# Kernel tuning notes

Hardware: AMD Instinct MI355X
Metric: run time of the kernel (lower is better)

The kernel has to match this reference:

```python
import jax, jax.numpy as jnp
import numpy as np

B, T, F = 32, 64, 128          # batch, time_steps, input_dim
H = 8                           # feat_dim (GRU hidden, MHA embed)
NH, HD = 4, 2                   # num_heads, head_dim
HID = 32                        # hidden_dim (out_proj out-features)


def setup_inputs() -> dict:
    key = jax.random.key(0)
    ks = jax.random.split(key, 16)
    s = 0.1
    inp = {
        'x': jax.random.normal(ks[0], (B, T, F), jnp.float32),
        # input_proj: Linear(F, F)
        'Wp': jax.random.normal(ks[1], (F, F), jnp.float32) * s,
        'bp': jax.random.normal(ks[2], (F,), jnp.float32) * s,
        # per-feature GRU weights stacked over F (input size 1 -> squeeze)
        'W_ih': jax.random.normal(ks[3], (F, 3 * H), jnp.float32) * s,
        'b_ih': jax.random.normal(ks[4], (F, 3 * H), jnp.float32) * s,
        'W_hh': jax.random.normal(ks[5], (F, 3 * H, H), jnp.float32) * s,
        'b_hh': jax.random.normal(ks[6], (F, 3 * H), jnp.float32) * s,
        # shared MultiheadAttention (embed=H, heads=NH)
        'in_w': jax.random.normal(ks[7], (3 * H, H), jnp.float32) * s,
        'in_b': jax.random.normal(ks[8], (3 * H,), jnp.float32) * s,
        'ow': jax.random.normal(ks[9], (H, H), jnp.float32) * s,
        'ob': jax.random.normal(ks[10], (H,), jnp.float32) * s,
        # out_proj: Linear(F*H, HID)
        'Wout': jax.random.normal(ks[11], (HID, F * H), jnp.float32) * s,
        'bout': jax.random.normal(ks[12], (HID,), jnp.float32) * s,
    }
    return inp


def _forward(x, Wp, bp, W_ih, b_ih, W_hh, b_hh, in_w, in_b, ow, ob, Wout, bout):
    xp = x @ Wp.T + bp                               # [B,T,F] input_proj

    # ---- batched per-feature GRU (vectorized over B and F, scan over T) ----
    def step(h, x_t):                                # h [B,F,H], x_t [B,F]
        gx = x_t[..., None] * W_ih + b_ih            # [B,F,3H]
        gh = jnp.einsum('bfh,fgh->bfg', h, W_hh) + b_hh
        r = jax.nn.sigmoid(gx[..., :H] + gh[..., :H])
        z = jax.nn.sigmoid(gx[..., H:2 * H] + gh[..., H:2 * H])
        n = jnp.tanh(gx[..., 2 * H:] + r * gh[..., 2 * H:])
        h_new = (1.0 - z) * n + z * h
        return h_new, h_new

    h0 = jnp.zeros((x.shape[0], F, H), x.dtype)
    _, hs = jax.lax.scan(step, h0, jnp.moveaxis(xp, 1, 0))   # [T,B,F,H]
    out = jnp.moveaxis(hs, 0, 1)                              # [B,T,F,H]

    # ---- shared MHA over time, batched across (B, F) ----
    seq = out.transpose(0, 2, 1, 3)                           # [B,F,T,H]
    qkv = seq @ in_w.T + in_b                                 # [B,F,T,3H]
    q, k, v = jnp.split(qkv, 3, axis=-1)
    def heads(t):  # [B,F,T,H] -> [B,F,T,NH,HD]
        return t.reshape(t.shape[:-1] + (NH, HD))
    q, k, v = heads(q), heads(k), heads(v)
    scale = 1.0 / np.sqrt(HD)
    scores = jnp.einsum('bfqnd,bfknd->bfnqk', q, k) * scale   # [B,F,NH,T,T]
    w = jax.nn.softmax(scores, axis=-1)
    ctx = jnp.einsum('bfnqk,bfknd->bfqnd', w, v)
    ctx = ctx.reshape(ctx.shape[:2] + (ctx.shape[2], H))      # [B,F,T,H]
    attn_out = ctx @ ow.T + ob                                # [B,F,T,H]
    attention = attn_out.transpose(0, 2, 1, 3)                # [B,T,F,H]

    # ---- flatten GRU outputs and project ----
    y = out.reshape(out.shape[0], out.shape[1], F * H) @ Wout.T + bout  # [B,T,HID]
    return y, attention


def reference(x, Wp, bp, W_ih, b_ih, W_hh, b_hh, in_w, in_b, ow, ob, Wout, bout):
    return _forward(x, Wp, bp, W_ih, b_ih, W_hh, b_hh, in_w, in_b, ow, ob, Wout, bout)
```

## Files before the change

### kernel.cpp

```cpp
#include <hip/hip_runtime.h>


namespace {
constexpr int Bb = 32, Tt = 64, Ff = 128, Hh = 8, HIDh = 32;
constexpr int G3H = 24;
constexpr float L2E = 1.44269504088896340736f;
constexpr int XS_STRIDE = 130;
constexpr int XP_OFF = Tt * XS_STRIDE;
constexpr int SMEM_AB = XP_OFF + 8 * 65;
constexpr int KK0 = 0, KK1 = 272, VV0 = 544, VV1 = 816, QS = 1088;
constexpr int WREG = 1728;
constexpr int OCT = 4 * WREG;
constexpr int SMEM_MHA = OCT + 4 * 640;
}

__device__ __forceinline__ float rcp_(float x) {
#if __has_builtin(__builtin_amdgcn_rcpf)
  return __builtin_amdgcn_rcpf(x);
#else
  return 1.0f / x;
#endif
}
__device__ __forceinline__ float exp2_(float x) {
#if __has_builtin(__builtin_amdgcn_exp2f)
  return __builtin_amdgcn_exp2f(x);
#else
  return exp2f(x);
#endif
}

__global__ __launch_bounds__(256) void k_gruproj(
    const float* __restrict__ x, const float* __restrict__ Wp, const float* __restrict__ bp,
    const float* __restrict__ W_ih, const float* __restrict__ b_ih,
    const float* __restrict__ W_hh, const float* __restrict__ b_hh,
    float* __restrict__ outp) {
  __shared__ float smem[SMEM_AB];
  const int tid = threadIdx.x;
  const int blk = blockIdx.x;
  const int b = blk >> 4;
  const int f0 = (blk & 15) * 8;
  const int lane = tid & 63;
  const int w = tid >> 6;

  {
    const float2* xb = (const float2*)(x + b * Tt * Ff);
    for (int i = tid; i < Tt * Ff / 2; i += 256) {
      int row = i >> 6, col2 = i & 63;
      *(float2*)&smem[row * XS_STRIDE + col2 * 2] = xb[i];
    }
  }
  __syncthreads();
  {
    const int t = lane;
    const int fA = f0 + w, fB = f0 + w + 4;
    float acc0 = bp[fA], acc1 = bp[fB];
    const float* wA = Wp + fA * Ff;
    const float* wB = Wp + fB * Ff;
    const float* xr = &smem[t * XS_STRIDE];
#pragma unroll 8
    for (int k = 0; k < Ff; k += 2) {
      float2 xv = *(const float2*)&xr[k];
      acc0 = fmaf(xv.x, wA[k], acc0); acc0 = fmaf(xv.y, wA[k + 1], acc0);
      acc1 = fmaf(xv.x, wB[k], acc1); acc1 = fmaf(xv.y, wB[k + 1], acc1);
    }
    smem[XP_OFF + w * 65 + t] = acc0;
    smem[XP_OFF + (w + 4) * 65 + t] = acc1;
  }
  __syncthreads();
  if (tid >= 64) return;

  {
    const int g = tid >> 3, j = tid & 7;
    const int f = f0 + g;
    const float* wb = W_hh + (f * G3H + j) * Hh;
    const float nL = -L2E, S2 = 2.0f * L2E;
    float w0s[8], w1s[8], w2s[8];
#pragma unroll
    for (int h = 0; h < 8; ++h) {
      w0s[h] = wb[h] * nL;
      w1s[h] = wb[64 + h] * nL;
      w2s[h] = wb[128 + h] * S2;
    }
    const float wi0s = W_ih[f * G3H + j] * nL;
    const float wi1s = W_ih[f * G3H + 8 + j] * nL;
    const float wi2s = W_ih[f * G3H + 16 + j] * S2;
    const float bias_r = (b_ih[f * G3H + j] + b_hh[f * G3H + j]) * nL;
    const float bias_z = (b_ih[f * G3H + 8 + j] + b_hh[f * G3H + 8 + j]) * nL;
    const float bi2s = b_ih[f * G3H + 16 + j] * S2;
    const float bh2s = b_hh[f * G3H + 16 + j] * S2;
    float hall[8];
#pragma unroll
    for (int h = 0; h < 8; ++h) hall[h] = 0.f;
    const int base = tid & 56;
    float* hdst = &smem[g * 520 + j * 65];
    const float* xps = &smem[XP_OFF + g * 65];
    for (int t = 0; t < Tt; ++t) {
      float xt = xps[t];
      float a0 = bias_r, a1 = bias_z, a2 = bh2s;
#pragma unroll
      for (int h = 0; h < 8; ++h) {
        a0 = fmaf(hall[h], w0s[h], a0);
        a1 = fmaf(hall[h], w1s[h], a1);
        a2 = fmaf(hall[h], w2s[h], a2);
      }
      float r = rcp_(1.0f + exp2_(fmaf(xt, wi0s, a0)));
      float z = rcp_(1.0f + exp2_(fmaf(xt, wi1s, a1)));
      float narg = fmaf(r, a2, fmaf(xt, wi2s, bi2s));
      float n = fmaf(-2.0f, rcp_(exp2_(narg) + 1.0f), 1.0f);
      float hn = fmaf(z, hall[j] - n, n);
      hdst[t] = hn;
#pragma unroll
      for (int h = 0; h < 8; ++h) hall[h] = __shfl(hn, base + h, 64);
    }
  }
  {
    float4* og = (float4*)(outp + (b * Ff + f0) * Tt * Hh);
#pragma unroll
    for (int i = 0; i < 16; ++i) {
      int v = i * 64 + tid;
      int g = v >> 7;
      int rem = v & 127;
      int t = rem >> 1, j0 = (rem & 1) * 4;
      const float* hp = &smem[g * 520 + j0 * 65 + t];
      og[v] = make_float4(hp[0], hp[65], hp[130], hp[195]);
    }
  }
}

#define MHA_STEP(K0C, K1C, V0C, V1C)                         \
  {                                                          \
    _Pragma("unroll") for (int i = 0; i < 4; ++i) {          \
      float s = fmaf(q0[i], K0C, q1[i] * K1C);               \
      float p = exp2_(s);                                    \
      ps[i] += p;                                            \
      c0[i] = fmaf(p, V0C, c0[i]);                           \
      c1[i] = fmaf(p, V1C, c1[i]);                           \
    }                                                        \
  }

__global__ __launch_bounds__(256) void k_mha_outproj(
    const float* __restrict__ outp, const float* __restrict__ in_w,
    const float* __restrict__ in_b, const float* __restrict__ ow,
    const float* __restrict__ ob, const float* __restrict__ Wout,
    const float* __restrict__ bout, float* __restrict__ attn,
    float* __restrict__ y) {
  __shared__ float smem[SMEM_MHA];
  const int tid = threadIdx.x;
  if (blockIdx.x < 1024) {
    const int wv = tid >> 6;
    const int t = tid & 63;
    const int pair = blockIdx.x * 4 + wv;
    float* sm = &smem[wv * WREG];

    const float4* src = (const float4*)(outp + pair * (Tt * Hh));
    float4 r0 = src[t * 2], r1 = src[t * 2 + 1];
    float sq[8] = {r0.x, r0.y, r0.z, r0.w, r1.x, r1.y, r1.z, r1.w};
    constexpr float SCL = 0.70710678118654752f * L2E;
    float qv[8], ka[8], va[8];
#pragma unroll
    for (int jj = 0; jj < 8; ++jj) {
      float aq = in_b[jj], ak = in_b[8 + jj], av = in_b[16 + jj];
#pragma unroll
      for (int h = 0; h < 8; ++h) {
        aq = fmaf(sq[h], in_w[jj * 8 + h], aq);
        ak = fmaf(sq[h], in_w[(8 + jj) * 8 + h], ak);
        av = fmaf(sq[h], in_w[(16 + jj) * 8 + h], av);
      }
      qv[jj] = aq * SCL; ka[jj] = ak; va[jj] = av;
    }
#pragma unroll
    for (int n = 0; n < 4; ++n) {
      *(float2*)&sm[QS + t * 10 + 2 * n] = make_float2(qv[2 * n], qv[2 * n + 1]);
      sm[KK0 + n * 68 + t] = ka[2 * n];
      sm[KK1 + n * 68 + t] = ka[2 * n + 1];
      sm[VV0 + n * 68 + t] = va[2 * n];
      sm[VV1 + n * 68 + t] = va[2 * n + 1];
    }
    asm volatile("s_waitcnt lgkmcnt(0)" ::: "memory");

    const int n = t >> 4, qq = t & 15;
    float q0[4], q1[4];
#pragma unroll
    for (int i = 0; i < 4; ++i) {
      float2 qp = *(const float2*)&sm[QS + (qq + 16 * i) * 10 + 2 * n];
      q0[i] = qp.x; q1[i] = qp.y;
    }
    float ps[4], c0[4], c1[4];
#pragma unroll
    for (int i = 0; i < 4; ++i) { ps[i] = 0.f; c0[i] = 0.f; c1[i] = 0.f; }
#pragma unroll 2
    for (int kt4 = 0; kt4 < Tt; kt4 += 4) {
      float4 k0 = *(const float4*)&sm[KK0 + n * 68 + kt4];
      float4 k1 = *(const float4*)&sm[KK1 + n * 68 + kt4];
      float4 v0 = *(const float4*)&sm[VV0 + n * 68 + kt4];
      float4 v1 = *(const float4*)&sm[VV1 + n * 68 + kt4];
      MHA_STEP(k0.x, k1.x, v0.x, v1.x)
      MHA_STEP(k0.y, k1.y, v0.y, v1.y)
      MHA_STEP(k0.z, k1.z, v0.z, v1.z)
      MHA_STEP(k0.w, k1.w, v0.w, v1.w)
    }
#pragma unroll
    for (int i = 0; i < 4; ++i) {
      float inv = rcp_(ps[i]);
      *(float2*)&sm[QS + (qq + 16 * i) * 10 + 2 * n] =
          make_float2(c0[i] * inv, c1[i] * inv);
    }
    asm volatile("s_waitcnt lgkmcnt(0)" ::: "memory");

    {
      float2 cp0 = *(const float2*)&sm[QS + t * 10 + 0];
      float2 cp1 = *(const float2*)&sm[QS + t * 10 + 2];
      float2 cp2 = *(const float2*)&sm[QS + t * 10 + 4];
      float2 cp3 = *(const float2*)&sm[QS + t * 10 + 6];
      float cx[8] = {cp0.x, cp0.y, cp1.x, cp1.y, cp2.x, cp2.y, cp3.x, cp3.y};
      float o8[8];
#pragma unroll
      for (int jj = 0; jj < 8; ++jj) {
        float a = ob[jj];
#pragma unroll
        for (int h = 0; h < 8; ++h) a = fmaf(cx[h], ow[jj * 8 + h], a);
        o8[jj] = a;
      }
      float* od = &smem[OCT + wv * 640 + t * 10];
      *(float4*)&od[0] = make_float4(o8[0], o8[1], o8[2], o8[3]);
      *(float4*)&od[4] = make_float4(o8[4], o8[5], o8[6], o8[7]);
    }
    __syncthreads();

    {
      const int bt = tid >> 2;
      const int c = tid & 3;
      const int b = blockIdx.x >> 5;
      const int f0 = (blockIdx.x & 31) * 4;
      const float* sp = &smem[OCT + c * 640 + bt * 10];
      float4* dst = (float4*)(attn + ((b * Tt + bt) * Ff + f0 + c) * Hh);
      dst[0] = *(const float4*)&sp[0];
      dst[1] = *(const float4*)&sp[4];
    }
  } else {
    constexpr int TT = 8;
    const int sub = tid >> 7, stid = tid & 127;
    const int eblk = (blockIdx.x - 1024) * 2 + sub;
    const int b = eblk >> 3;
    const int t0 = (eblk & 7) * TT;
    const int oq = stid >> 4;
    const int fc = stid & 15;
    float acc[TT][4];
#pragma unroll
    for (int tt = 0; tt < TT; ++tt)
#pragma unroll
      for (int od = 0; od < 4; ++od) acc[tt][od] = 0.f;
#pragma unroll
    for (int ff = 0; ff < 8; ++ff) {
      int f = fc * 8 + ff;
      const float4* rb = (const float4*)(outp + ((b * Ff + f) * Tt + t0) * Hh);
      float4 rv[16];
#pragma unroll
      for (int i = 0; i < 16; ++i) rv[i] = rb[i];
#pragma unroll
      for (int od = 0; od < 4; ++od) {
        int o = oq * 4 + od;
        const float4* wbp = (const float4*)(Wout + o * (Ff * Hh) + f * Hh);
        float4 wa = wbp[0], wc = wbp[1];
#pragma unroll
        for (int tt = 0; tt < TT; ++tt) {
          float4 ra = rv[tt * 2], rc = rv[tt * 2 + 1];
          float s = acc[tt][od];
          s = fmaf(ra.x, wa.x, s); s = fmaf(ra.y, wa.y, s);
          s = fmaf(ra.z, wa.z, s); s = fmaf(ra.w, wa.w, s);
          s = fmaf(rc.x, wc.x, s); s = fmaf(rc.y, wc.y, s);
          s = fmaf(rc.z, wc.z, s); s = fmaf(rc.w, wc.w, s);
          acc[tt][od] = s;
        }
      }
    }
#pragma unroll
    for (int tt = 0; tt < TT; ++tt)
#pragma unroll
      for (int od = 0; od < 4; ++od) {
        float v = acc[tt][od];
        v += __shfl_xor(v, 1, 16);
        v += __shfl_xor(v, 2, 16);
        v += __shfl_xor(v, 4, 16);
        v += __shfl_xor(v, 8, 16);
        acc[tt][od] = v;
      }
#pragma unroll
    for (int tt = 0; tt < TT; ++tt) {
      if (fc == tt) {
#pragma unroll
        for (int od = 0; od < 4; ++od) {
          int o = oq * 4 + od;
          y[(b * Tt + t0 + tt) * HIDh + o] = acc[tt][od] + bout[o];
        }
      }
    }
  }
}

extern "C" void kernel_launch(void* const* d_in, const int* in_sizes, int n_in,
                              void* d_out, int out_size, void* d_ws, size_t ws_size,
                              hipStream_t stream) {
  (void)in_sizes; (void)n_in; (void)out_size; (void)ws_size;
  const float* x    = (const float*)d_in[0];
  const float* Wp   = (const float*)d_in[1];
  const float* bp   = (const float*)d_in[2];
  const float* W_ih = (const float*)d_in[3];
  const float* b_ih = (const float*)d_in[4];
  const float* W_hh = (const float*)d_in[5];
  const float* b_hh = (const float*)d_in[6];
  const float* in_w = (const float*)d_in[7];
  const float* in_b = (const float*)d_in[8];
  const float* ow   = (const float*)d_in[9];
  const float* ob   = (const float*)d_in[10];
  const float* Wout = (const float*)d_in[11];
  const float* bout = (const float*)d_in[12];

  float* y    = (float*)d_out;
  float* attn = (float*)d_out + Bb * Tt * HIDh;
  float* outp = (float*)d_ws;

  hipLaunchKernelGGL(k_gruproj, dim3(Bb * (Ff / 8)), dim3(256), 0, stream,
                     x, Wp, bp, W_ih, b_ih, W_hh, b_hh, outp);
  hipLaunchKernelGGL(k_mha_outproj, dim3(1152), dim3(256), 0, stream,
                     outp, in_w, in_b, ow, ob, Wout, bout, attn, y);
}
```

Baseline: 65.48 us.

## Fuse MHA into GRU kernel using shared-memory hidden states, split out_proj

Each GRU block now runs the shared multi-head attention for its 8 features straight from the hidden-state history held in shared memory, with all four waves taking part after the recurrence. This removes the round trip through the workspace for the attention path. The output projection moves to its own small kernel. The GRU wave gets raised priority and the block uses more shared memory, which may limit occupancy. The attention work is now serialized behind the GRU inside each block rather than spread across a separate wide grid.

```diff
diff --git a/kernel.cpp b/kernel.cpp
--- a/kernel.cpp
+++ b/kernel.cpp
@@ -6,12 +6,11 @@
 constexpr int G3H = 24;
 constexpr float L2E = 1.44269504088896340736f;
 constexpr int XS_STRIDE = 130;
-constexpr int XP_OFF = Tt * XS_STRIDE;
-constexpr int SMEM_AB = XP_OFF + 8 * 65;
+constexpr int XP = 8320;
+constexpr int OCT = 4160;
+constexpr int WKV = 9280;
 constexpr int KK0 = 0, KK1 = 272, VV0 = 544, VV1 = 816, QS = 1088;
-constexpr int WREG = 1728;
-constexpr int OCT = 4 * WREG;
-constexpr int SMEM_MHA = OCT + 4 * 640;
+constexpr int SM_SIZE = 16192;
 }
 
 __device__ __forceinline__ float rcp_(float x) {
@@ -29,12 +28,25 @@
 #endif
 }
 
-__global__ __launch_bounds__(256) void k_gruproj(
+#define MHA_STEP(K0C, K1C, V0C, V1C)                         \
+  {                                                          \
+    _Pragma("unroll") for (int i = 0; i < 4; ++i) {          \
+      float s = fmaf(q0[i], K0C, q1[i] * K1C);               \
+      float p = exp2_(s);                                    \
+      ps[i] += p;                                            \
+      c0[i] = fmaf(p, V0C, c0[i]);                           \
+      c1[i] = fmaf(p, V1C, c1[i]);                           \
+    }                                                        \
+  }
+
+__global__ __launch_bounds__(256, 2) void k_fused(
     const float* __restrict__ x, const float* __restrict__ Wp, const float* __restrict__ bp,
     const float* __restrict__ W_ih, const float* __restrict__ b_ih,
     const float* __restrict__ W_hh, const float* __restrict__ b_hh,
-    float* __restrict__ outp) {
-  __shared__ float smem[SMEM_AB];
+    const float* __restrict__ in_w, const float* __restrict__ in_b,
+    const float* __restrict__ ow, const float* __restrict__ ob,
+    float* __restrict__ outp, float* __restrict__ attn) {
+  __shared__ float smem[SM_SIZE];
   const int tid = threadIdx.x;
   const int blk = blockIdx.x;
   const int b = blk >> 4;
@@ -63,13 +75,13 @@
       acc0 = fmaf(xv.x, wA[k], acc0); acc0 = fmaf(xv.y, wA[k + 1], acc0);
       acc1 = fmaf(xv.x, wB[k], acc1); acc1 = fmaf(xv.y, wB[k + 1], acc1);
     }
-    smem[XP_OFF + w * 65 + t] = acc0;
-    smem[XP_OFF + (w + 4) * 65 + t] = acc1;
+    smem[XP + w * 65 + t] = acc0;
+    smem[XP + (w + 4) * 65 + t] = acc1;
   }
   __syncthreads();
-  if (tid >= 64) return;
-
-  {
+
+  if (tid < 64) {
+    __builtin_amdgcn_s_setprio(1);
     const int g = tid >> 3, j = tid & 7;
     const int f = f0 + g;
     const float* wb = W_hh + (f * G3H + j) * Hh;
@@ -93,7 +105,7 @@
     for (int h = 0; h < 8; ++h) hall[h] = 0.f;
     const int base = tid & 56;
     float* hdst = &smem[g * 520 + j * 65];
-    const float* xps = &smem[XP_OFF + g * 65];
+    const float* xps = &smem[XP + g * 65];
     for (int t = 0; t < Tt; ++t) {
       float xt = xps[t];
       float a0 = bias_r, a1 = bias_z, a2 = bh2s;
@@ -112,12 +124,15 @@
 #pragma unroll
       for (int h = 0; h < 8; ++h) hall[h] = __shfl(hn, base + h, 64);
     }
-  }
+    __builtin_amdgcn_s_setprio(0);
+  }
+  __syncthreads();
+
   {
     float4* og = (float4*)(outp + (b * Ff + f0) * Tt * Hh);
 #pragma unroll
-    for (int i = 0; i < 16; ++i) {
-      int v = i * 64 + tid;
+    for (int i = 0; i < 4; ++i) {
+      int v = i * 256 + tid;
       int g = v >> 7;
       int rem = v & 127;
       int t = rem >> 1, j0 = (rem & 1) * 4;
@@ -125,174 +140,160 @@
       og[v] = make_float4(hp[0], hp[65], hp[130], hp[195]);
     }
   }
-}
-
-#define MHA_STEP(K0C, K1C, V0C, V1C)                         \
-  {                                                          \
-    _Pragma("unroll") for (int i = 0; i < 4; ++i) {          \
-      float s = fmaf(q0[i], K0C, q1[i] * K1C);               \
-      float p = exp2_(s);                                    \
-      ps[i] += p;                                            \
-      c0[i] = fmaf(p, V0C, c0[i]);                           \
-      c1[i] = fmaf(p, V1C, c1[i]);                           \
-    }                                                        \
-  }
-
-__global__ __launch_bounds__(256) void k_mha_outproj(
-    const float* __restrict__ outp, const float* __restrict__ in_w,
-    const float* __restrict__ in_b, const float* __restrict__ ow,
-    const float* __restrict__ ob, const float* __restrict__ Wout,
-    const float* __restrict__ bout, float* __restrict__ attn,
-    float* __restrict__ y) {
-  __shared__ float smem[SMEM_MHA];
-  const int tid = threadIdx.x;
-  if (blockIdx.x < 1024) {
-    const int wv = tid >> 6;
-    const int t = tid & 63;
-    const int pair = blockIdx.x * 4 + wv;
-    float* sm = &smem[wv * WREG];
-
-    const float4* src = (const float4*)(outp + pair * (Tt * Hh));
-    float4 r0 = src[t * 2], r1 = src[t * 2 + 1];
-    float sq[8] = {r0.x, r0.y, r0.z, r0.w, r1.x, r1.y, r1.z, r1.w};
+
+  {
+    const int t = lane;
+    float* sm = &smem[WKV + w * 1728];
     constexpr float SCL = 0.70710678118654752f * L2E;
-    float qv[8], ka[8], va[8];
-#pragma unroll
-    for (int jj = 0; jj < 8; ++jj) {
-      float aq = in_b[jj], ak = in_b[8 + jj], av = in_b[16 + jj];
-#pragma unroll
-      for (int h = 0; h < 8; ++h) {
-        aq = fmaf(sq[h], in_w[jj * 8 + h], aq);
-        ak = fmaf(sq[h], in_w[(8 + jj) * 8 + h], ak);
-        av = fmaf(sq[h], in_w[(16 + jj) * 8 + h], av);
-      }
-      qv[jj] = aq * SCL; ka[jj] = ak; va[jj] = av;
-    }
-#pragma unroll
-    for (int n = 0; n < 4; ++n) {
-      *(float2*)&sm[QS + t * 10 + 2 * n] = make_float2(qv[2 * n], qv[2 * n + 1]);
-      sm[KK0 + n * 68 + t] = ka[2 * n];
-      sm[KK1 + n * 68 + t] = ka[2 * n + 1];
-      sm[VV0 + n * 68 + t] = va[2 * n];
-      sm[VV1 + n * 68 + t] = va[2 * n + 1];
-    }
-    asm volatile("s_waitcnt lgkmcnt(0)" ::: "memory");
-
-    const int n = t >> 4, qq = t & 15;
-    float q0[4], q1[4];
+#pragma unroll
+    for (int fl = w; fl < 8; fl += 4) {
+      const float* hsrc = &smem[fl * 520];
+      float sq[8];
+#pragma unroll
+      for (int h = 0; h < 8; ++h) sq[h] = hsrc[h * 65 + t];
+      float qv[8], ka[8], va[8];
+#pragma unroll
+      for (int jj = 0; jj < 8; ++jj) {
+        float aq = in_b[jj], ak = in_b[8 + jj], av = in_b[16 + jj];
+#pragma unroll
+        for (int h = 0; h < 8; ++h) {
+          aq = fmaf(sq[h], in_w[jj * 8 + h], aq);
+          ak = fmaf(sq[h], in_w[(8 + jj) * 8 + h], ak);
+          av = fmaf(sq[h], in_w[(16 + jj) * 8 + h], av);
+        }
+        qv[jj] = aq * SCL; ka[jj] = ak; va[jj] = av;
+      }
+#pragma unroll
+      for (int n = 0; n < 4; ++n) {
+        *(float2*)&sm[QS + t * 10 + 2 * n] = make_float2(qv[2 * n], qv[2 * n + 1]);
+        sm[KK0 + n * 68 + t] = ka[2 * n];
+        sm[KK1 + n * 68 + t] = ka[2 * n + 1];
+        sm[VV0 + n * 68 + t] = va[2 * n];
+        sm[VV1 + n * 68 + t] = va[2 * n + 1];
+      }
+      asm volatile("s_waitcnt lgkmcnt(0)" ::: "memory");
+
+      const int n = t >> 4, qq = t & 15;
+      float q0[4], q1[4];
+#pragma unroll
+      for (int i = 0; i < 4; ++i) {
+        float2 qp = *(const float2*)&sm[QS + (qq + 16 * i) * 10 + 2 * n];
+        q0[i] = qp.x; q1[i] = qp.y;
+      }
+      float ps[4], c0[4], c1[4];
+#pragma unroll
+      for (int i = 0; i < 4; ++i) { ps[i] = 0.f; c0[i] = 0.f; c1[i] = 0.f; }
+#pragma unroll 2
+      for (int kt4 = 0; kt4 < Tt; kt4 += 4) {
+        float4 k0 = *(const float4*)&sm[KK0 + n * 68 + kt4];
+        float4 k1 = *(const float4*)&sm[KK1 + n * 68 + kt4];
+        float4 v0 = *(const float4*)&sm[VV0 + n * 68 + kt4];
+        float4 v1 = *(const float4*)&sm[VV1 + n * 68 + kt4];
+        MHA_STEP(k0.x, k1.x, v0.x, v1.x)
+        MHA_STEP(k0.y, k1.y, v0.y, v1.y)
+        MHA_STEP(k0.z, k1.z, v0.z, v1.z)
+        MHA_STEP(k0.w, k1.w, v0.w, v1.w)
+      }
+#pragma unroll
+      for (int i = 0; i < 4; ++i) {
+        float inv = rcp_(ps[i]);
+        *(float2*)&sm[QS + (qq + 16 * i) * 10 + 2 * n] =
+            make_float2(c0[i] * inv, c1[i] * inv);
+      }
+      asm volatile("s_waitcnt lgkmcnt(0)" ::: "memory");
+
+      {
+        float2 cp0 = *(const float2*)&sm[QS + t * 10 + 0];
+        float2 cp1 = *(const float2*)&sm[QS + t * 10 + 2];
+        float2 cp2 = *(const float2*)&sm[QS + t * 10 + 4];
+        float2 cp3 = *(const float2*)&sm[QS + t * 10 + 6];
+        float cx[8] = {cp0.x, cp0.y, cp1.x, cp1.y, cp2.x, cp2.y, cp3.x, cp3.y};
+        float o8[8];
+#pragma unroll
+        for (int jj = 0; jj < 8; ++jj) {
+          float a = ob[jj];
+#pragma unroll
+          for (int h = 0; h < 8; ++h) a = fmaf(cx[h], ow[jj * 8 + h], a);
+          o8[jj] = a;
+        }
+        float* od = &smem[OCT + fl * 640 + t * 10];
+        *(float4*)&od[0] = make_float4(o8[0], o8[1], o8[2], o8[3]);
+        *(float4*)&od[4] = make_float4(o8[4], o8[5], o8[6], o8[7]);
+      }
+    }
+  }
+  __syncthreads();
+
+  {
 #pragma unroll
     for (int i = 0; i < 4; ++i) {
-      float2 qp = *(const float2*)&sm[QS + (qq + 16 * i) * 10 + 2 * n];
-      q0[i] = qp.x; q1[i] = qp.y;
-    }
-    float ps[4], c0[4], c1[4];
-#pragma unroll
-    for (int i = 0; i < 4; ++i) { ps[i] = 0.f; c0[i] = 0.f; c1[i] = 0.f; }
-#pragma unroll 2
-    for (int kt4 = 0; kt4 < Tt; kt4 += 4) {
-      float4 k0 = *(const float4*)&sm[KK0 + n * 68 + kt4];
-      float4 k1 = *(const float4*)&sm[KK1 + n * 68 + kt4];
-      float4 v0 = *(const float4*)&sm[VV0 + n * 68 + kt4];
-      float4 v1 = *(const float4*)&sm[VV1 + n * 68 + kt4];
-      MHA_STEP(k0.x, k1.x, v0.x, v1.x)
-      MHA_STEP(k0.y, k1.y, v0.y, v1.y)
-      MHA_STEP(k0.z, k1.z, v0.z, v1.z)
-      MHA_STEP(k0.w, k1.w, v0.w, v1.w)
-    }
-#pragma unroll
-    for (int i = 0; i < 4; ++i) {
-      float inv = rcp_(ps[i]);
-      *(float2*)&sm[QS + (qq + 16 * i) * 10 + 2 * n] =
-          make_float2(c0[i] * inv, c1[i] * inv);
-    }
-    asm volatile("s_waitcnt lgkmcnt(0)" ::: "memory");
-
-    {
-      float2 cp0 = *(const float2*)&sm[QS + t * 10 + 0];
-      float2 cp1 = *(const float2*)&sm[QS + t * 10 + 2];
-      float2 cp2 = *(const float2*)&sm[QS + t * 10 + 4];
-      float2 cp3 = *(const float2*)&sm[QS + t * 10 + 6];
-      float cx[8] = {cp0.x, cp0.y, cp1.x, cp1.y, cp2.x, cp2.y, cp3.x, cp3.y};
-      float o8[8];
-#pragma unroll
-      for (int jj = 0; jj < 8; ++jj) {
-        float a = ob[jj];
-#pragma unroll
-        for (int h = 0; h < 8; ++h) a = fmaf(cx[h], ow[jj * 8 + h], a);
-        o8[jj] = a;
-      }
-      float* od = &smem[OCT + wv * 640 + t * 10];
-      *(float4*)&od[0] = make_float4(o8[0], o8[1], o8[2], o8[3]);
-      *(float4*)&od[4] = make_float4(o8[4], o8[5], o8[6], o8[7]);
-    }
-    __syncthreads();
-
-    {
-      const int bt = tid >> 2;
-      const int c = tid & 3;
-      const int b = blockIdx.x >> 5;
-      const int f0 = (blockIdx.x & 31) * 4;
-      const float* sp = &smem[OCT + c * 640 + bt * 10];
-      float4* dst = (float4*)(attn + ((b * Tt + bt) * Ff + f0 + c) * Hh);
-      dst[0] = *(const float4*)&sp[0];
-      dst[1] = *(const float4*)&sp[4];
-    }
-  } else {
-    constexpr int TT = 8;
-    const int sub = tid >> 7, stid = tid & 127;
-    const int eblk = (blockIdx.x - 1024) * 2 + sub;
-    const int b = eblk >> 3;
-    const int t0 = (eblk & 7) * TT;
-    const int oq = stid >> 4;
-    const int fc = stid & 15;
-    float acc[TT][4];
-#pragma unroll
-    for (int tt = 0; tt < TT; ++tt)
-#pragma unroll
-      for (int od = 0; od < 4; ++od) acc[tt][od] = 0.f;
-#pragma unroll
-    for (int ff = 0; ff < 8; ++ff) {
-      int f = fc * 8 + ff;
-      const float4* rb = (const float4*)(outp + ((b * Ff + f) * Tt + t0) * Hh);
-      float4 rv[16];
-#pragma unroll
-      for (int i = 0; i < 16; ++i) rv[i] = rb[i];
+      int v = i * 256 + tid;
+      int t = v >> 4;
+      int c = v & 15;
+      const float* sp = &smem[OCT + (c >> 1) * 640 + t * 10 + (c & 1) * 4];
+      float4* dst = (float4*)(attn + ((b * Tt + t) * Ff + f0) * Hh);
+      dst[v & 15 ? c : c] = *(const float4*)sp;
+    }
+  }
+}
+
+__global__ __launch_bounds__(128) void k_outproj(
+    const float* __restrict__ outp, const float* __restrict__ Wout,
+    const float* __restrict__ bout, float* __restrict__ y) {
+  constexpr int TT = 8;
+  int blk = blockIdx.x;
+  int b = blk >> 3;
+  int t0 = (blk & 7) * TT;
+  int tid = threadIdx.x;
+  int oq = tid >> 4;
+  int fc = tid & 15;
+  float acc[TT][4];
+#pragma unroll
+  for (int tt = 0; tt < TT; ++tt)
+#pragma unroll
+    for (int od = 0; od < 4; ++od) acc[tt][od] = 0.f;
+#pragma unroll
+  for (int ff = 0; ff < 8; ++ff) {
+    int f = fc * 8 + ff;
+    const float4* rb = (const float4*)(outp + ((b * Ff + f) * Tt + t0) * Hh);
+    float4 rv[16];
+#pragma unroll
+    for (int i = 0; i < 16; ++i) rv[i] = rb[i];
+#pragma unroll
+    for (int od = 0; od < 4; ++od) {
+      int o = oq * 4 + od;
+      const float4* wbp = (const float4*)(Wout + o * (Ff * Hh) + f * Hh);
+      float4 wa = wbp[0], wc = wbp[1];
+#pragma unroll
+      for (int tt = 0; tt < TT; ++tt) {
+        float4 ra = rv[tt * 2], rc = rv[tt * 2 + 1];
+        float s = acc[tt][od];
+        s = fmaf(ra.x, wa.x, s); s = fmaf(ra.y, wa.y, s);
+        s = fmaf(ra.z, wa.z, s); s = fmaf(ra.w, wa.w, s);
+        s = fmaf(rc.x, wc.x, s); s = fmaf(rc.y, wc.y, s);
+        s = fmaf(rc.z, wc.z, s); s = fmaf(rc.w, wc.w, s);
+        acc[tt][od] = s;
+      }
+    }
+  }
+#pragma unroll
+  for (int tt = 0; tt < TT; ++tt)
+#pragma unroll
+    for (int od = 0; od < 4; ++od) {
+      float v = acc[tt][od];
+      v += __shfl_xor(v, 1, 16);
+      v += __shfl_xor(v, 2, 16);
+      v += __shfl_xor(v, 4, 16);
+      v += __shfl_xor(v, 8, 16);
+      acc[tt][od] = v;
+    }
+#pragma unroll
+  for (int tt = 0; tt < TT; ++tt) {
+    if (fc == tt) {
 #pragma unroll
       for (int od = 0; od < 4; ++od) {
         int o = oq * 4 + od;
-        const float4* wbp = (const float4*)(Wout + o * (Ff * Hh) + f * Hh);
-        float4 wa = wbp[0], wc = wbp[1];
-#pragma unroll
-        for (int tt = 0; tt < TT; ++tt) {
-          float4 ra = rv[tt * 2], rc = rv[tt * 2 + 1];
-          float s = acc[tt][od];
-          s = fmaf(ra.x, wa.x, s); s = fmaf(ra.y, wa.y, s);
-          s = fmaf(ra.z, wa.z, s); s = fmaf(ra.w, wa.w, s);
-          s = fmaf(rc.x, wc.x, s); s = fmaf(rc.y, wc.y, s);
-          s = fmaf(rc.z, wc.z, s); s = fmaf(rc.w, wc.w, s);
-          acc[tt][od] = s;
-        }
-      }
-    }
-#pragma unroll
-    for (int tt = 0; tt < TT; ++tt)
-#pragma unroll
-      for (int od = 0; od < 4; ++od) {
-        float v = acc[tt][od];
-        v += __shfl_xor(v, 1, 16);
-        v += __shfl_xor(v, 2, 16);
-        v += __shfl_xor(v, 4, 16);
-        v += __shfl_xor(v, 8, 16);
-        acc[tt][od] = v;
-      }
-#pragma unroll
-    for (int tt = 0; tt < TT; ++tt) {
-      if (fc == tt) {
-#pragma unroll
-        for (int od = 0; od < 4; ++od) {
-          int o = oq * 4 + od;
-          y[(b * Tt + t0 + tt) * HIDh + o] = acc[tt][od] + bout[o];
-        }
+        y[(b * Tt + t0 + tt) * HIDh + o] = acc[tt][od] + bout[o];
       }
     }
   }
@@ -320,8 +321,8 @@
   float* attn = (float*)d_out + Bb * Tt * HIDh;
   float* outp = (float*)d_ws;
 
-  hipLaunchKernelGGL(k_gruproj, dim3(Bb * (Ff / 8)), dim3(256), 0, stream,
-                     x, Wp, bp, W_ih, b_ih, W_hh, b_hh, outp);
-  hipLaunchKernelGGL(k_mha_outproj, dim3(1152), dim3(256), 0, stream,
-                     outp, in_w, in_b, ow, ob, Wout, bout, attn, y);
-}
+  hipLaunchKernelGGL(k_fused, dim3(Bb * (Ff / 8)), dim3(256), 0, stream,
+                     x, Wp, bp, W_ih, b_ih, W_hh, b_hh, in_w, in_b, ow, ob, outp, attn);
+  hipLaunchKernelGGL(k_outproj, dim3(Bb * (Tt / 8)), dim3(128), 0, stream,
+                     outp, Wout, bout, y);
+}
```

Result: faster. 56.89 us (-13.1%).
